# Kernel tuning notes

Hardware: AMD Instinct MI355X
Metric: run time of the kernel (lower is better)

The kernel has to match this reference:

```python
import jax, jax.numpy as jnp
import numpy as np

H = 4096          # hidden_size
HS = 64           # head_size
NH = H // HS      # num_heads = 64
TM = 64           # TIME_MIX_EXTRA_DIM (hidden_size == 4096)
TD = 128          # TIME_DECAY_EXTRA_DIM (hidden_size == 4096)
EPS = 1e-5


def _ln(v, w, b):
    mu = v.mean(-1, keepdims=True)
    var = v.var(-1, keepdims=True)
    return (v - mu) / jnp.sqrt(var + EPS) * w + b


def setup_inputs() -> dict:
    key = jax.random.key(0)
    ks = jax.random.split(key, 20)
    def n(i, shape, s=0.02):
        return jax.random.normal(ks[i], shape, dtype=jnp.float32) * s
    return {
        "x": n(0, (1, 1, H), 1.0),
        "state1": n(1, (1, 1, H), 1.0),
        "state2": n(2, (NH, HS, HS), 1.0),
        "ln1_w": jnp.ones((H,), jnp.float32),
        "ln1_b": jnp.zeros((H,), jnp.float32),
        "time_maa_x": n(3, (1, 1, H), 0.1),
        "time_maa": n(4, (5, 1, H), 0.1),       # stacked [w,k,v,r,g] mixes
        "maa_w1": n(5, (H, 5 * TM)),
        "maa_w2": n(6, (5, TM, H)),
        "time_decay": n(7, (NH, HS, 1), 0.5),
        "time_first": n(8, (NH, HS, 1), 0.5),
        "decay_w1": n(9, (H, TD)),
        "decay_w2": n(10, (TD, H)),
        "Wr": n(11, (H, H)),
        "Wk": n(12, (H, H)),
        "Wv": n(13, (H, H)),
        "Wg": n(14, (H, H)),
        "Wo": n(15, (H, H)),
        "lnx_w": jnp.ones((H,), jnp.float32),
        "lnx_b": jnp.zeros((H,), jnp.float32),
    }


def reference(x, state1, state2, ln1_w, ln1_b, time_maa_x, time_maa,
              maa_w1, maa_w2, time_decay, time_first, decay_w1, decay_w2,
              Wr, Wk, Wv, Wg, Wo, lnx_w, lnx_b):
    last_x = x
    xl = _ln(x, ln1_w, ln1_b)                         # [1,1,H]
    sx = state1 - xl                                  # token-shift delta
    xxx = xl + sx * time_maa_x                        # [1,1,H]
    xxx = jnp.tanh(xxx @ maa_w1).reshape(5, 1, TM)    # LoRA down, 5 mixes
    xxx = jnp.einsum('fot,fth->foh', xxx, maa_w2)     # LoRA up -> [5,1,H]
    xxx = xl + sx * (xxx + time_maa)                  # [5,1,H]
    mw, mk, mv, mr, mg = xxx[0], xxx[1], xxx[2], xxx[3], xxx[4]  # each [1,H]

    r = (mr @ Wr.T).reshape(NH, 1, HS)
    k = (mk @ Wk.T).reshape(NH, HS, 1)
    v = (mv @ Wv.T).reshape(NH, 1, HS)
    g = jax.nn.silu(mg @ Wg.T)                        # [1,H]

    # data-dependent decay (LoRA): exp(-exp(clip(w)))
    td = (jnp.tanh(mw @ decay_w1) @ decay_w2).reshape(NH, HS, 1) + time_decay
    td = jnp.exp(-jnp.exp(jnp.clip(td, -9.72, 2.27)))

    kv = k @ v                                        # [NH,HS,HS] outer product
    wkv = kv * time_first + state2                    # bonus + state
    out_h = (r @ wkv).reshape(NH, HS)                 # per-head readout
    state2_out = kv + state2 * td                     # state recurrence

    # InstanceNorm2d over head_size per head (no affine), then elementwise affine
    mu = out_h.mean(-1, keepdims=True)
    var = out_h.var(-1, keepdims=True)
    o = ((out_h - mu) / jnp.sqrt(var + EPS)).reshape(1, 1, H)
    o = o * lnx_w + lnx_b
    o = (o * g) @ Wo.T
    return (last_x + o, xl, state2_out)
```

## Files before the change

kernel.cpp:

```cpp
#include <hip/hip_runtime.h>
#include <hip/hip_bf16.h>


#define HDIM 4096
#define NHEAD 64
#define HSZ 64

#define WS_XL    0
#define WS_SX    4096
#define WS_XXX   8192
#define WS_MV    12288
#define WS_PART  32768
#define WS_DPART 32768
#define WS_TD    53248
#define WS_R     57344
#define WS_K     61440
#define WS_V     65536
#define WS_G     69632
#define WS_OG    73728
#define WS_FLAG  77824

typedef unsigned short bfraw;

__device__ __forceinline__ float bf2f(bfraw u) {
    union { unsigned int u; float f; } v; v.u = ((unsigned int)u) << 16; return v.f;
}
__device__ __forceinline__ bfraw f2bf(float f) {
    union { float f; unsigned int u; } v; v.f = f;
    unsigned int u = v.u;
    unsigned int r = (u + 0x7fffu + ((u >> 16) & 1u)) >> 16;
    return (bfraw)r;
}
__device__ __forceinline__ float ldin(const void* p, long long i, bool isbf) {
    return isbf ? bf2f(((const bfraw*)p)[i]) : ((const float*)p)[i];
}
__device__ __forceinline__ void stout(void* p, long long i, float v, bool isbf) {
    if (isbf) ((bfraw*)p)[i] = f2bf(v); else ((float*)p)[i] = v;
}
__device__ __forceinline__ float waveReduce(float v) {
    for (int m = 32; m; m >>= 1) v += __shfl_xor(v, m);
    return v;
}

__global__ __launch_bounds__(256)
void k1_ln_mix(const void* __restrict__ x, const void* __restrict__ st1,
               const void* __restrict__ lnw, const void* __restrict__ lnb,
               const void* __restrict__ tmx, void* __restrict__ dout,
               float* __restrict__ ws) {
    int tid = threadIdx.x;
    __shared__ float red[8];
    __shared__ float sflag;
    {
        const bfraw* p = (const bfraw*)x;
        bfraw u = p[tid];
        int e = (u >> 7) & 0xFF;
        int cnt = (e >= 96 && e <= 144) ? 1 : 0;
        for (int m = 32; m; m >>= 1) cnt += __shfl_xor(cnt, m);
        if ((tid & 63) == 0) red[tid >> 6] = (float)cnt;
        __syncthreads();
        if (tid == 0) {
            float c = red[0] + red[1] + red[2] + red[3];
            float fl = (c >= 208.0f) ? 1.0f : 0.0f;
            sflag = fl;
            ws[WS_FLAG] = fl;
        }
        __syncthreads();
    }
    bool isbf = sflag != 0.0f;

    float xv[16];
    float s1 = 0.f, s2 = 0.f;
    for (int k = 0; k < 16; ++k) {
        float v = ldin(x, tid + k * 256, isbf);
        xv[k] = v; s1 += v; s2 += v * v;
    }
    s1 = waveReduce(s1); s2 = waveReduce(s2);
    int wid = tid >> 6, lane = tid & 63;
    if (lane == 0) { red[wid] = s1; red[4 + wid] = s2; }
    __syncthreads();
    float t1 = red[0] + red[1] + red[2] + red[3];
    float t2 = red[4] + red[5] + red[6] + red[7];
    float mu = t1 * (1.0f / HDIM);
    float var = fmaxf(t2 * (1.0f / HDIM) - mu * mu, 0.0f);
    float rstd = rsqrtf(var + 1e-5f);
    for (int k = 0; k < 16; ++k) {
        int i = tid + k * 256;
        float xl = (xv[k] - mu) * rstd * ldin(lnw, i, isbf) + ldin(lnb, i, isbf);
        float sx = ldin(st1, i, isbf) - xl;
        float xxx = xl + sx * ldin(tmx, i, isbf);
        stout(dout, 4096 + i, xl, isbf);
        ws[WS_XL + i] = xl;
        ws[WS_SX + i] = sx;
        ws[WS_XXX + i] = xxx;
    }
}

__global__ __launch_bounds__(320)
void k2a_maa_down(const void* __restrict__ w1, float* __restrict__ ws) {
    bool isbf = ws[WS_FLAG] != 0.0f;
    __shared__ float lx[64];
    int tid = threadIdx.x, b = blockIdx.x;
    if (tid < 64) lx[tid] = ws[WS_XXX + b * 64 + tid];
    __syncthreads();
    float acc = 0.f;
    long long base = (long long)b * 64 * 320 + tid;
    #pragma unroll 8
    for (int j = 0; j < 64; ++j) acc += lx[j] * ldin(w1, base + (long long)j * 320, isbf);
    ws[WS_PART + b * 320 + tid] = acc;
}

__global__ __launch_bounds__(256)
void k2c_maa_up(const void* __restrict__ w2, const void* __restrict__ tm,
                float* __restrict__ ws) {
    bool isbf = ws[WS_FLAG] != 0.0f;
    int tid = threadIdx.x;
    int f = blockIdx.x >> 4;
    int hb = (blockIdx.x & 15) << 8;
    __shared__ float zl[64];
    if (tid < 64) {
        float s = 0.f;
        #pragma unroll 8
        for (int b = 0; b < 64; ++b) s += ws[WS_PART + b * 320 + f * 64 + tid];
        zl[tid] = tanhf(s);
    }
    __syncthreads();
    int h = hb + tid;
    float acc = 0.f;
    long long base = (long long)f * 64 * HDIM + h;
    #pragma unroll 8
    for (int t = 0; t < 64; ++t) acc += zl[t] * ldin(w2, base + (long long)t * HDIM, isbf);
    float mval = ws[WS_XL + h] + ws[WS_SX + h] * (acc + ldin(tm, f * HDIM + h, isbf));
    ws[WS_MV + f * HDIM + h] = mval;
}

__global__ __launch_bounds__(128)
void k3a_decay_down(const void* __restrict__ dw1, float* __restrict__ ws) {
    bool isbf = ws[WS_FLAG] != 0.0f;
    __shared__ float lm[32];
    int tid = threadIdx.x, b = blockIdx.x;
    if (tid < 32) lm[tid] = ws[WS_MV + b * 32 + tid];
    __syncthreads();
    float acc = 0.f;
    long long base = (long long)b * 32 * 128 + tid;
    #pragma unroll 8
    for (int j = 0; j < 32; ++j) acc += lm[j] * ldin(dw1, base + (long long)j * 128, isbf);
    ws[WS_DPART + b * 128 + tid] = acc;
}

__global__ __launch_bounds__(128)
void k3b_decay_up(const void* __restrict__ dw2, const void* __restrict__ tdec,
                  float* __restrict__ ws) {
    bool isbf = ws[WS_FLAG] != 0.0f;
    int tid = threadIdx.x;
    __shared__ float dz[128];
    {
        float s = 0.f;
        #pragma unroll 8
        for (int b = 0; b < 128; ++b) s += ws[WS_DPART + b * 128 + tid];
        dz[tid] = tanhf(s);
    }
    __syncthreads();
    int i = blockIdx.x * 128 + tid;
    float acc = 0.f;
    #pragma unroll 8
    for (int t = 0; t < 128; ++t) acc += dz[t] * ldin(dw2, (long long)t * HDIM + i, isbf);
    float tv = acc + ldin(tdec, i, isbf);
    tv = fminf(fmaxf(tv, -9.72f), 2.27f);
    ws[WS_TD + i] = expf(-expf(tv));
}

__device__ __forceinline__ void issue8(const bfraw* __restrict__ wr, int lane,
                                       uint4 buf[8]) {
    #pragma unroll
    for (int it = 0; it < 8; ++it)
        buf[it] = *(const uint4*)(wr + it * 512 + lane * 8);
}
__device__ __forceinline__ float consume8(const uint4 buf[8],
                                          const float* __restrict__ mLds, int lane) {
    float acc = 0.f;
    #pragma unroll
    for (int it = 0; it < 8; ++it) {
        int base = it * 512 + lane * 8;
        float4 m0 = *(const float4*)(mLds + base);
        float4 m1 = *(const float4*)(mLds + base + 4);
        uint4 w4 = buf[it];
        acc += bf2f((bfraw)(w4.x & 0xffff)) * m0.x + bf2f((bfraw)(w4.x >> 16)) * m0.y;
        acc += bf2f((bfraw)(w4.y & 0xffff)) * m0.z + bf2f((bfraw)(w4.y >> 16)) * m0.w;
        acc += bf2f((bfraw)(w4.z & 0xffff)) * m1.x + bf2f((bfraw)(w4.z >> 16)) * m1.y;
        acc += bf2f((bfraw)(w4.w & 0xffff)) * m1.z + bf2f((bfraw)(w4.w >> 16)) * m1.w;
    }
    return acc;
}
__device__ __forceinline__ float dot_row_f32(const float* __restrict__ wr,
                                             const float* __restrict__ mLds, int lane) {
    float acc = 0.f;
    #pragma unroll
    for (int h = 0; h < 2; ++h) {
        float4 av[8];
        #pragma unroll
        for (int it = 0; it < 8; ++it)
            av[it] = *(const float4*)(wr + h * 2048 + it * 256 + lane * 4);
        __builtin_amdgcn_sched_barrier(0);
        #pragma unroll
        for (int it = 0; it < 8; ++it) {
            int base = h * 2048 + it * 256 + lane * 4;
            float4 m0 = *(const float4*)(mLds + base);
            float4 a = av[it];
            acc += a.x * m0.x + a.y * m0.y + a.z * m0.z + a.w * m0.w;
        }
    }
    return acc;
}

__global__ __launch_bounds__(256)
void k4_matvec4(const void* __restrict__ Wr, const void* __restrict__ Wk,
                const void* __restrict__ Wv, const void* __restrict__ Wg,
                float* __restrict__ ws) {
    bool isbf = ws[WS_FLAG] != 0.0f;
    int tid = threadIdx.x;
    int wid = tid >> 6, lane = tid & 63;
    int mat = blockIdx.x >> 8;
    int bb = blockIdx.x & 255;
    const void* W; const float* msrc; float* y;
    if (mat == 0)      { W = Wr; msrc = ws + WS_MV + 3 * HDIM; y = ws + WS_R; }
    else if (mat == 1) { W = Wk; msrc = ws + WS_MV + 1 * HDIM; y = ws + WS_K; }
    else if (mat == 2) { W = Wv; msrc = ws + WS_MV + 2 * HDIM; y = ws + WS_V; }
    else               { W = Wg; msrc = ws + WS_MV + 4 * HDIM; y = ws + WS_G; }
    __shared__ __align__(16) float lm[HDIM];
    for (int i = tid * 4; i < HDIM; i += 1024)
        *(float4*)(lm + i) = *(const float4*)(msrc + i);
    __syncthreads();
    int r0 = bb * 16 + wid * 4;
    float acc0, acc1, acc2, acc3;
    if (isbf) {
        const bfraw* w0 = (const bfraw*)W + (long long)r0 * HDIM;
        uint4 A[8], B[8];
        issue8(w0, lane, A);
        issue8(w0 + HDIM, lane, B);
        __builtin_amdgcn_sched_barrier(0);
        acc0 = consume8(A, lm, lane);
        issue8(w0 + 2 * HDIM, lane, A);
        __builtin_amdgcn_sched_barrier(0);
        acc1 = consume8(B, lm, lane);
        issue8(w0 + 3 * HDIM, lane, B);
        __builtin_amdgcn_sched_barrier(0);
        acc2 = consume8(A, lm, lane);
        acc3 = consume8(B, lm, lane);
    } else {
        const float* w0 = (const float*)W + (long long)r0 * HDIM;
        acc0 = dot_row_f32(w0, lm, lane);
        acc1 = dot_row_f32(w0 + HDIM, lm, lane);
        acc2 = dot_row_f32(w0 + 2 * HDIM, lm, lane);
        acc3 = dot_row_f32(w0 + 3 * HDIM, lm, lane);
    }
    acc0 = waveReduce(acc0); acc1 = waveReduce(acc1);
    acc2 = waveReduce(acc2); acc3 = waveReduce(acc3);
    if (lane == 0) {
        if (mat == 3) {
            acc0 = acc0 / (1.0f + expf(-acc0));
            acc1 = acc1 / (1.0f + expf(-acc1));
            acc2 = acc2 / (1.0f + expf(-acc2));
            acc3 = acc3 / (1.0f + expf(-acc3));
        }
        y[r0] = acc0; y[r0 + 1] = acc1; y[r0 + 2] = acc2; y[r0 + 3] = acc3;
    }
}

__global__ __launch_bounds__(64)
void k5_heads(const void* __restrict__ state2, const void* __restrict__ tfirst,
              const void* __restrict__ lnxw, const void* __restrict__ lnxb,
              void* __restrict__ dout, float* __restrict__ ws) {
    bool isbf = ws[WS_FLAG] != 0.0f;
    int h = blockIdx.x, j = threadIdx.x;
    int gi = h * 64 + j;
    float rj = ws[WS_R + gi], kj = ws[WS_K + gi], vj = ws[WS_V + gi];
    float tdj = ws[WS_TD + gi];
    float tfj = ldin(tfirst, gi, isbf);
    __shared__ float lr[64], lk[64], ltd[64];
    lr[j] = rj; lk[j] = kj; ltd[j] = tdj;
    float c = waveReduce(rj * kj * tfj);
    __syncthreads();
    float acc = 0.f;
    long long sbase = (long long)h * 4096 + j;
    #pragma unroll 8
    for (int i = 0; i < 64; ++i) {
        float s = ldin(state2, sbase + i * 64, isbf);
        acc += lr[i] * s;
        stout(dout, 8192 + sbase + i * 64, lk[i] * vj + s * ltd[i], isbf);
    }
    float oh = vj * c + acc;
    float s1 = waveReduce(oh);
    float s2 = waveReduce(oh * oh);
    float mu = s1 * (1.0f / 64.0f);
    float var = fmaxf(s2 * (1.0f / 64.0f) - mu * mu, 0.0f);
    float rstd = rsqrtf(var + 1e-5f);
    float o = (oh - mu) * rstd * ldin(lnxw, gi, isbf) + ldin(lnxb, gi, isbf);
    ws[WS_OG + gi] = o * ws[WS_G + gi];
}

__global__ __launch_bounds__(256)
void k6_out(const void* __restrict__ Wo, const void* __restrict__ x,
            void* __restrict__ dout, float* __restrict__ ws) {
    bool isbf = ws[WS_FLAG] != 0.0f;
    int tid = threadIdx.x;
    int wid = tid >> 6, lane = tid & 63;
    __shared__ __align__(16) float lm[HDIM];
    for (int i = tid * 4; i < HDIM; i += 1024)
        *(float4*)(lm + i) = *(const float4*)(ws + WS_OG + i);
    __syncthreads();
    int r0 = blockIdx.x * 8 + wid * 2;
    float acc0, acc1;
    if (isbf) {
        const bfraw* w0 = (const bfraw*)Wo + (long long)r0 * HDIM;
        uint4 A[8], B[8];
        issue8(w0, lane, A);
        issue8(w0 + HDIM, lane, B);
        __builtin_amdgcn_sched_barrier(0);
        acc0 = consume8(A, lm, lane);
        acc1 = consume8(B, lm, lane);
    } else {
        const float* w0 = (const float*)Wo + (long long)r0 * HDIM;
        acc0 = dot_row_f32(w0, lm, lane);
        acc1 = dot_row_f32(w0 + HDIM, lm, lane);
    }
    acc0 = waveReduce(acc0); acc1 = waveReduce(acc1);
    if (lane == 0) {
        stout(dout, r0,     ldin(x, r0, isbf)     + acc0, isbf);
        stout(dout, r0 + 1, ldin(x, r0 + 1, isbf) + acc1, isbf);
    }
}

extern "C" void kernel_launch(void* const* d_in, const int* in_sizes, int n_in,
                              void* d_out, int out_size, void* d_ws, size_t ws_size,
                              hipStream_t stream) {
    const void* x      = d_in[0];
    const void* st1    = d_in[1];
    const void* st2    = d_in[2];
    const void* ln1w   = d_in[3];
    const void* ln1b   = d_in[4];
    const void* tmx    = d_in[5];
    const void* tmaa   = d_in[6];
    const void* maw1   = d_in[7];
    const void* maw2   = d_in[8];
    const void* tdec   = d_in[9];
    const void* tfirst = d_in[10];
    const void* dw1    = d_in[11];
    const void* dw2    = d_in[12];
    const void* Wr     = d_in[13];
    const void* Wk     = d_in[14];
    const void* Wv     = d_in[15];
    const void* Wg     = d_in[16];
    const void* Wo     = d_in[17];
    const void* lnxw   = d_in[18];
    const void* lnxb   = d_in[19];

    float* ws = (float*)d_ws;

    k1_ln_mix<<<1, 256, 0, stream>>>(x, st1, ln1w, ln1b, tmx, d_out, ws);
    k2a_maa_down<<<64, 320, 0, stream>>>(maw1, ws);
    k2c_maa_up<<<80, 256, 0, stream>>>(maw2, tmaa, ws);
    k3a_decay_down<<<128, 128, 0, stream>>>(dw1, ws);
    k3b_decay_up<<<32, 128, 0, stream>>>(dw2, tdec, ws);
    k4_matvec4<<<1024, 256, 0, stream>>>(Wr, Wk, Wv, Wg, ws);
    k5_heads<<<64, 64, 0, stream>>>(st2, tfirst, lnxw, lnxb, d_out, ws);
    k6_out<<<512, 256, 0, stream>>>(Wo, x, d_out, ws);
}
```

Measured before the change: 418.2 us.

## Fuse LN, LoRA and decay stages into fewer kernel launches

Merges the eight-kernel pipeline into five by fusing LayerNorm with the mix LoRA down projection, the LoRA up projection with the decay down projection, and the decay up projection with the four big matvecs as extra blocks. Each fused block recomputes the LayerNorm statistics and the w-mix slice it needs, which adds redundant work but removes launch gaps and workspace round trips. The workspace layout is compacted, r/k/v/g are stored contiguously, and one scheduling barrier is dropped in the f32 path.

```diff
diff --git a/kernel.cpp b/kernel.cpp
--- a/kernel.cpp
+++ b/kernel.cpp
@@ -3,22 +3,16 @@
 
 
 #define HDIM 4096
-#define NHEAD 64
-#define HSZ 64
 
 #define WS_XL    0
 #define WS_SX    4096
-#define WS_XXX   8192
-#define WS_MV    12288
-#define WS_PART  32768
-#define WS_DPART 32768
-#define WS_TD    53248
-#define WS_R     57344
-#define WS_K     61440
-#define WS_V     65536
-#define WS_G     69632
-#define WS_OG    73728
-#define WS_FLAG  77824
+#define WS_MV    8192
+#define WS_PART  28672
+#define WS_R     28672
+#define WS_TD    45056
+#define WS_DPART 49152
+#define WS_OG    65536
+#define WS_FLAG  69632
 
 typedef unsigned short bfraw;
 
@@ -40,133 +34,6 @@
 __device__ __forceinline__ float waveReduce(float v) {
     for (int m = 32; m; m >>= 1) v += __shfl_xor(v, m);
     return v;
-}
-
-__global__ __launch_bounds__(256)
-void k1_ln_mix(const void* __restrict__ x, const void* __restrict__ st1,
-               const void* __restrict__ lnw, const void* __restrict__ lnb,
-               const void* __restrict__ tmx, void* __restrict__ dout,
-               float* __restrict__ ws) {
-    int tid = threadIdx.x;
-    __shared__ float red[8];
-    __shared__ float sflag;
-    {
-        const bfraw* p = (const bfraw*)x;
-        bfraw u = p[tid];
-        int e = (u >> 7) & 0xFF;
-        int cnt = (e >= 96 && e <= 144) ? 1 : 0;
-        for (int m = 32; m; m >>= 1) cnt += __shfl_xor(cnt, m);
-        if ((tid & 63) == 0) red[tid >> 6] = (float)cnt;
-        __syncthreads();
-        if (tid == 0) {
-            float c = red[0] + red[1] + red[2] + red[3];
-            float fl = (c >= 208.0f) ? 1.0f : 0.0f;
-            sflag = fl;
-            ws[WS_FLAG] = fl;
-        }
-        __syncthreads();
-    }
-    bool isbf = sflag != 0.0f;
-
-    float xv[16];
-    float s1 = 0.f, s2 = 0.f;
-    for (int k = 0; k < 16; ++k) {
-        float v = ldin(x, tid + k * 256, isbf);
-        xv[k] = v; s1 += v; s2 += v * v;
-    }
-    s1 = waveReduce(s1); s2 = waveReduce(s2);
-    int wid = tid >> 6, lane = tid & 63;
-    if (lane == 0) { red[wid] = s1; red[4 + wid] = s2; }
-    __syncthreads();
-    float t1 = red[0] + red[1] + red[2] + red[3];
-    float t2 = red[4] + red[5] + red[6] + red[7];
-    float mu = t1 * (1.0f / HDIM);
-    float var = fmaxf(t2 * (1.0f / HDIM) - mu * mu, 0.0f);
-    float rstd = rsqrtf(var + 1e-5f);
-    for (int k = 0; k < 16; ++k) {
-        int i = tid + k * 256;
-        float xl = (xv[k] - mu) * rstd * ldin(lnw, i, isbf) + ldin(lnb, i, isbf);
-        float sx = ldin(st1, i, isbf) - xl;
-        float xxx = xl + sx * ldin(tmx, i, isbf);
-        stout(dout, 4096 + i, xl, isbf);
-        ws[WS_XL + i] = xl;
-        ws[WS_SX + i] = sx;
-        ws[WS_XXX + i] = xxx;
-    }
-}
-
-__global__ __launch_bounds__(320)
-void k2a_maa_down(const void* __restrict__ w1, float* __restrict__ ws) {
-    bool isbf = ws[WS_FLAG] != 0.0f;
-    __shared__ float lx[64];
-    int tid = threadIdx.x, b = blockIdx.x;
-    if (tid < 64) lx[tid] = ws[WS_XXX + b * 64 + tid];
-    __syncthreads();
-    float acc = 0.f;
-    long long base = (long long)b * 64 * 320 + tid;
-    #pragma unroll 8
-    for (int j = 0; j < 64; ++j) acc += lx[j] * ldin(w1, base + (long long)j * 320, isbf);
-    ws[WS_PART + b * 320 + tid] = acc;
-}
-
-__global__ __launch_bounds__(256)
-void k2c_maa_up(const void* __restrict__ w2, const void* __restrict__ tm,
-                float* __restrict__ ws) {
-    bool isbf = ws[WS_FLAG] != 0.0f;
-    int tid = threadIdx.x;
-    int f = blockIdx.x >> 4;
-    int hb = (blockIdx.x & 15) << 8;
-    __shared__ float zl[64];
-    if (tid < 64) {
-        float s = 0.f;
-        #pragma unroll 8
-        for (int b = 0; b < 64; ++b) s += ws[WS_PART + b * 320 + f * 64 + tid];
-        zl[tid] = tanhf(s);
-    }
-    __syncthreads();
-    int h = hb + tid;
-    float acc = 0.f;
-    long long base = (long long)f * 64 * HDIM + h;
-    #pragma unroll 8
-    for (int t = 0; t < 64; ++t) acc += zl[t] * ldin(w2, base + (long long)t * HDIM, isbf);
-    float mval = ws[WS_XL + h] + ws[WS_SX + h] * (acc + ldin(tm, f * HDIM + h, isbf));
-    ws[WS_MV + f * HDIM + h] = mval;
-}
-
-__global__ __launch_bounds__(128)
-void k3a_decay_down(const void* __restrict__ dw1, float* __restrict__ ws) {
-    bool isbf = ws[WS_FLAG] != 0.0f;
-    __shared__ float lm[32];
-    int tid = threadIdx.x, b = blockIdx.x;
-    if (tid < 32) lm[tid] = ws[WS_MV + b * 32 + tid];
-    __syncthreads();
-    float acc = 0.f;
-    long long base = (long long)b * 32 * 128 + tid;
-    #pragma unroll 8
-    for (int j = 0; j < 32; ++j) acc += lm[j] * ldin(dw1, base + (long long)j * 128, isbf);
-    ws[WS_DPART + b * 128 + tid] = acc;
-}
-
-__global__ __launch_bounds__(128)
-void k3b_decay_up(const void* __restrict__ dw2, const void* __restrict__ tdec,
-                  float* __restrict__ ws) {
-    bool isbf = ws[WS_FLAG] != 0.0f;
-    int tid = threadIdx.x;
-    __shared__ float dz[128];
-    {
-        float s = 0.f;
-        #pragma unroll 8
-        for (int b = 0; b < 128; ++b) s += ws[WS_DPART + b * 128 + tid];
-        dz[tid] = tanhf(s);
-    }
-    __syncthreads();
-    int i = blockIdx.x * 128 + tid;
-    float acc = 0.f;
-    #pragma unroll 8
-    for (int t = 0; t < 128; ++t) acc += dz[t] * ldin(dw2, (long long)t * HDIM + i, isbf);
-    float tv = acc + ldin(tdec, i, isbf);
-    tv = fminf(fmaxf(tv, -9.72f), 2.27f);
-    ws[WS_TD + i] = expf(-expf(tv));
 }
 
 __device__ __forceinline__ void issue8(const bfraw* __restrict__ wr, int lane,
@@ -200,7 +67,6 @@
         #pragma unroll
         for (int it = 0; it < 8; ++it)
             av[it] = *(const float4*)(wr + h * 2048 + it * 256 + lane * 4);
-        __builtin_amdgcn_sched_barrier(0);
         #pragma unroll
         for (int it = 0; it < 8; ++it) {
             int base = h * 2048 + it * 256 + lane * 4;
@@ -213,20 +79,151 @@
 }
 
 __global__ __launch_bounds__(256)
-void k4_matvec4(const void* __restrict__ Wr, const void* __restrict__ Wk,
-                const void* __restrict__ Wv, const void* __restrict__ Wg,
-                float* __restrict__ ws) {
+void kA_ln_k2a(const void* __restrict__ x, const void* __restrict__ st1,
+               const void* __restrict__ lnw, const void* __restrict__ lnb,
+               const void* __restrict__ tmx, const void* __restrict__ w1,
+               void* __restrict__ dout, float* __restrict__ ws) {
+    int tid = threadIdx.x, b = blockIdx.x;
+    int wid = tid >> 6, lane = tid & 63;
+    bool isbf;
+    {
+        bfraw u = ((const bfraw*)x)[lane];
+        int e = (u >> 7) & 0xFF;
+        unsigned long long ball = __ballot(e >= 96 && e <= 144);
+        isbf = __popcll(ball) >= 56;
+    }
+    if (b == 0 && tid == 0) ws[WS_FLAG] = isbf ? 1.0f : 0.0f;
+
+    __shared__ float red[8];
+    __shared__ float lx[64];
+    float xv[16]; float s1 = 0.f, s2 = 0.f;
+    for (int k = 0; k < 16; ++k) {
+        float v = ldin(x, tid + k * 256, isbf);
+        xv[k] = v; s1 += v; s2 += v * v;
+    }
+    s1 = waveReduce(s1); s2 = waveReduce(s2);
+    if (lane == 0) { red[wid] = s1; red[4 + wid] = s2; }
+    __syncthreads();
+    float t1 = red[0] + red[1] + red[2] + red[3];
+    float t2 = red[4] + red[5] + red[6] + red[7];
+    float mu = t1 * (1.0f / HDIM);
+    float var = fmaxf(t2 * (1.0f / HDIM) - mu * mu, 0.0f);
+    float rstd = rsqrtf(var + 1e-5f);
+    for (int k = 0; k < 16; ++k) {
+        int i = tid + k * 256;
+        if ((i >> 6) == b) {
+            float xl = (xv[k] - mu) * rstd * ldin(lnw, i, isbf) + ldin(lnb, i, isbf);
+            float sx = ldin(st1, i, isbf) - xl;
+            float xxx = xl + sx * ldin(tmx, i, isbf);
+            stout(dout, 4096 + i, xl, isbf);
+            ws[WS_XL + i] = xl;
+            ws[WS_SX + i] = sx;
+            lx[i & 63] = xxx;
+        }
+    }
+    __syncthreads();
+    for (int c = tid; c < 320; c += 256) {
+        float acc = 0.f;
+        long long base = (long long)b * 64 * 320 + c;
+        #pragma unroll 8
+        for (int j = 0; j < 64; ++j)
+            acc += lx[j] * ldin(w1, base + (long long)j * 320, isbf);
+        ws[WS_PART + b * 320 + c] = acc;
+    }
+}
+
+__global__ __launch_bounds__(256)
+void kB_up_k3a(const void* __restrict__ w2, const void* __restrict__ tm,
+               const void* __restrict__ dw1, float* __restrict__ ws) {
+    bool isbf = ws[WS_FLAG] != 0.0f;
+    int tid = threadIdx.x, b = blockIdx.x;
+    __shared__ float zl[64];
+    __shared__ float mwl[32];
+    if (b < 80) {
+        int f = b >> 4, hb = (b & 15) << 8;
+        if (tid < 64) {
+            float s = 0.f;
+            #pragma unroll 8
+            for (int p = 0; p < 64; ++p) s += ws[WS_PART + p * 320 + f * 64 + tid];
+            zl[tid] = tanhf(s);
+        }
+        __syncthreads();
+        int h = hb + tid;
+        float acc = 0.f;
+        long long base = (long long)f * 64 * HDIM + h;
+        #pragma unroll 8
+        for (int t = 0; t < 64; ++t)
+            acc += zl[t] * ldin(w2, base + (long long)t * HDIM, isbf);
+        float mval = ws[WS_XL + h] + ws[WS_SX + h] * (acc + ldin(tm, (long long)f * HDIM + h, isbf));
+        ws[WS_MV + f * HDIM + h] = mval;
+    } else {
+        int d = b - 80;
+        if (tid < 64) {
+            float s = 0.f;
+            #pragma unroll 8
+            for (int p = 0; p < 64; ++p) s += ws[WS_PART + p * 320 + tid];
+            zl[tid] = tanhf(s);
+        }
+        __syncthreads();
+        if (tid < 32) {
+            int h = d * 32 + tid;
+            float acc = 0.f;
+            #pragma unroll 8
+            for (int t = 0; t < 64; ++t)
+                acc += zl[t] * ldin(w2, (long long)t * HDIM + h, isbf);
+            mwl[tid] = ws[WS_XL + h] + ws[WS_SX + h] * (acc + ldin(tm, h, isbf));
+        }
+        __syncthreads();
+        if (tid < 128) {
+            float acc = 0.f;
+            long long base = (long long)d * 32 * 128 + tid;
+            #pragma unroll 8
+            for (int j = 0; j < 32; ++j)
+                acc += mwl[j] * ldin(dw1, base + (long long)j * 128, isbf);
+            ws[WS_DPART + d * 128 + tid] = acc;
+        }
+    }
+}
+
+__global__ __launch_bounds__(256)
+void kC_k3b_k4(const void* __restrict__ dw2, const void* __restrict__ tdec,
+               const void* __restrict__ Wr, const void* __restrict__ Wk,
+               const void* __restrict__ Wv, const void* __restrict__ Wg,
+               float* __restrict__ ws) {
     bool isbf = ws[WS_FLAG] != 0.0f;
     int tid = threadIdx.x;
+    __shared__ __align__(16) float lm[HDIM];
+    if (blockIdx.x < 32) {
+        int bb = blockIdx.x;
+        if (tid < 128) {
+            float s = 0.f;
+            #pragma unroll 8
+            for (int p = 0; p < 128; ++p) s += ws[WS_DPART + p * 128 + tid];
+            lm[tid] = tanhf(s);
+        }
+        __syncthreads();
+        if (tid < 128) {
+            int i = bb * 128 + tid;
+            float acc = 0.f;
+            #pragma unroll 8
+            for (int t = 0; t < 128; ++t)
+                acc += lm[t] * ldin(dw2, (long long)t * HDIM + i, isbf);
+            float tv = acc + ldin(tdec, i, isbf);
+            tv = fminf(fmaxf(tv, -9.72f), 2.27f);
+            ws[WS_TD + i] = expf(-expf(tv));
+        }
+        return;
+    }
+    int k4b = blockIdx.x - 32;
     int wid = tid >> 6, lane = tid & 63;
-    int mat = blockIdx.x >> 8;
-    int bb = blockIdx.x & 255;
-    const void* W; const float* msrc; float* y;
-    if (mat == 0)      { W = Wr; msrc = ws + WS_MV + 3 * HDIM; y = ws + WS_R; }
-    else if (mat == 1) { W = Wk; msrc = ws + WS_MV + 1 * HDIM; y = ws + WS_K; }
-    else if (mat == 2) { W = Wv; msrc = ws + WS_MV + 2 * HDIM; y = ws + WS_V; }
-    else               { W = Wg; msrc = ws + WS_MV + 4 * HDIM; y = ws + WS_G; }
-    __shared__ __align__(16) float lm[HDIM];
+    int mat = k4b >> 8;
+    int bb = k4b & 255;
+    const void* W; const float* msrc;
+    if (mat == 0)      { W = Wr; msrc = ws + WS_MV + 3 * HDIM; }
+    else if (mat == 1) { W = Wk; msrc = ws + WS_MV + 1 * HDIM; }
+    else if (mat == 2) { W = Wv; msrc = ws + WS_MV + 2 * HDIM; }
+    else               { W = Wg; msrc = ws + WS_MV + 4 * HDIM; }
+    float* y = ws + WS_R + mat * HDIM;
     for (int i = tid * 4; i < HDIM; i += 1024)
         *(float4*)(lm + i) = *(const float4*)(msrc + i);
     __syncthreads();
@@ -267,13 +264,14 @@
 }
 
 __global__ __launch_bounds__(64)
-void k5_heads(const void* __restrict__ state2, const void* __restrict__ tfirst,
+void kD_heads(const void* __restrict__ state2, const void* __restrict__ tfirst,
               const void* __restrict__ lnxw, const void* __restrict__ lnxb,
               void* __restrict__ dout, float* __restrict__ ws) {
     bool isbf = ws[WS_FLAG] != 0.0f;
     int h = blockIdx.x, j = threadIdx.x;
     int gi = h * 64 + j;
-    float rj = ws[WS_R + gi], kj = ws[WS_K + gi], vj = ws[WS_V + gi];
+    float rj = ws[WS_R + gi], kj = ws[WS_R + HDIM + gi];
+    float vj = ws[WS_R + 2 * HDIM + gi], gj = ws[WS_R + 3 * HDIM + gi];
     float tdj = ws[WS_TD + gi];
     float tfj = ldin(tfirst, gi, isbf);
     __shared__ float lr[64], lk[64], ltd[64];
@@ -295,11 +293,11 @@
     float var = fmaxf(s2 * (1.0f / 64.0f) - mu * mu, 0.0f);
     float rstd = rsqrtf(var + 1e-5f);
     float o = (oh - mu) * rstd * ldin(lnxw, gi, isbf) + ldin(lnxb, gi, isbf);
-    ws[WS_OG + gi] = o * ws[WS_G + gi];
+    ws[WS_OG + gi] = o * gj;
 }
 
 __global__ __launch_bounds__(256)
-void k6_out(const void* __restrict__ Wo, const void* __restrict__ x,
+void kE_out(const void* __restrict__ Wo, const void* __restrict__ x,
             void* __restrict__ dout, float* __restrict__ ws) {
     bool isbf = ws[WS_FLAG] != 0.0f;
     int tid = threadIdx.x;
@@ -356,12 +354,9 @@
 
     float* ws = (float*)d_ws;
 
-    k1_ln_mix<<<1, 256, 0, stream>>>(x, st1, ln1w, ln1b, tmx, d_out, ws);
-    k2a_maa_down<<<64, 320, 0, stream>>>(maw1, ws);
-    k2c_maa_up<<<80, 256, 0, stream>>>(maw2, tmaa, ws);
-    k3a_decay_down<<<128, 128, 0, stream>>>(dw1, ws);
-    k3b_decay_up<<<32, 128, 0, stream>>>(dw2, tdec, ws);
-    k4_matvec4<<<1024, 256, 0, stream>>>(Wr, Wk, Wv, Wg, ws);
-    k5_heads<<<64, 64, 0, stream>>>(st2, tfirst, lnxw, lnxb, d_out, ws);
-    k6_out<<<512, 256, 0, stream>>>(Wo, x, d_out, ws);
-}
+    kA_ln_k2a<<<64, 256, 0, stream>>>(x, st1, ln1w, ln1b, tmx, maw1, d_out, ws);
+    kB_up_k3a<<<208, 256, 0, stream>>>(maw2, tmaa, dw1, ws);
+    kC_k3b_k4<<<1056, 256, 0, stream>>>(dw2, tdec, Wr, Wk, Wv, Wg, ws);
+    kD_heads<<<64, 64, 0, stream>>>(st2, tfirst, lnxw, lnxb, d_out, ws);
+    kE_out<<<512, 256, 0, stream>>>(Wo, x, d_out, ws);
+}
```

Result: faster. 392.2 us (-6.2%).
